# Optimization experiments

Hardware: AMD Instinct MI355X
Metric: run time of the kernel (lower is better)

Reference implementation:

```python
import jax, jax.numpy as jnp
import numpy as np

N = 50000
E = 800000
F_IN = 128
HID = 128
H_HID = 4
H_OUT = 6
N_CLS = 40
NEG_SLOPE = 0.2
BN_EPS = 1e-5


def gat_conv(x, src, dst, W, a_src, a_dst, bias, concat):
    # x: [N, F_in]; W: [F_in, H*C]; a_src/a_dst: [H, C]
    H, C = a_src.shape
    h = (x @ W).reshape(N, H, C)                      # [N,H,C]
    alpha_s = jnp.sum(h * a_src[None], axis=-1)       # [N,H]
    alpha_d = jnp.sum(h * a_dst[None], axis=-1)       # [N,H]
    e = jax.nn.leaky_relu(alpha_s[src] + alpha_d[dst], NEG_SLOPE)  # [E',H]
    # segment softmax over incoming edges of each dst node
    emax = jax.ops.segment_max(e, dst, num_segments=N)
    e = jnp.exp(e - emax[dst])
    denom = jax.ops.segment_sum(e, dst, num_segments=N)
    alpha = e / (denom[dst] + 1e-16)                  # [E',H]
    out = jax.ops.segment_sum(alpha[:, :, None] * h[src], dst, num_segments=N)  # [N,H,C]
    out = out.reshape(N, H * C) if concat else out.mean(axis=1)
    return out + bias


def bn_eval(x, gamma, beta, mean, var):
    return (x - mean) * (gamma / jnp.sqrt(var + BN_EPS)) + beta


def setup_inputs() -> dict:
    key = jax.random.key(0)
    ks = jax.random.split(key, 24)
    d_h = HID * H_HID  # 512
    inp = {
        'x': jax.random.normal(ks[0], (N, F_IN), jnp.float32),
        'edge_index': jax.random.randint(ks[1], (2, E), 0, N, jnp.int64),
        # layer 0: GATConv(128 -> 128, heads=4, concat)
        'W0': jax.random.normal(ks[2], (F_IN, d_h), jnp.float32) * 0.1,
        'as0': jax.random.normal(ks[3], (H_HID, HID), jnp.float32) * 0.1,
        'ad0': jax.random.normal(ks[4], (H_HID, HID), jnp.float32) * 0.1,
        'b0': jnp.zeros((d_h,), jnp.float32),
        'g0': jax.random.uniform(ks[5], (d_h,), jnp.float32, 0.5, 1.5),
        'bt0': jax.random.normal(ks[6], (d_h,), jnp.float32) * 0.1,
        'm0': jax.random.normal(ks[7], (d_h,), jnp.float32) * 0.1,
        'v0': jax.random.uniform(ks[8], (d_h,), jnp.float32, 0.5, 1.5),
        # layer 1: GATConv(512 -> 128, heads=4, concat)
        'W1': jax.random.normal(ks[9], (d_h, d_h), jnp.float32) * 0.05,
        'as1': jax.random.normal(ks[10], (H_HID, HID), jnp.float32) * 0.1,
        'ad1': jax.random.normal(ks[11], (H_HID, HID), jnp.float32) * 0.1,
        'b1': jnp.zeros((d_h,), jnp.float32),
        'g1': jax.random.uniform(ks[12], (d_h,), jnp.float32, 0.5, 1.5),
        'bt1': jax.random.normal(ks[13], (d_h,), jnp.float32) * 0.1,
        'm1': jax.random.normal(ks[14], (d_h,), jnp.float32) * 0.1,
        'v1': jax.random.uniform(ks[15], (d_h,), jnp.float32, 0.5, 1.5),
        # layer 2: GATConv(512 -> 40, heads=6, concat=False)
        'W2': jax.random.normal(ks[16], (d_h, H_OUT * N_CLS), jnp.float32) * 0.05,
        'as2': jax.random.normal(ks[17], (H_OUT, N_CLS), jnp.float32) * 0.1,
        'ad2': jax.random.normal(ks[18], (H_OUT, N_CLS), jnp.float32) * 0.1,
        'b2': jnp.zeros((N_CLS,), jnp.float32),
    }
    return inp


def reference(x, edge_index, W0, as0, ad0, b0, g0, bt0, m0, v0,
              W1, as1, ad1, b1, g1, bt1, m1, v1,
              W2, as2, ad2, b2):
    # add self loops (PyG GATConv default add_self_loops=True)
    loop = jnp.arange(N, dtype=edge_index.dtype)
    src = jnp.concatenate([edge_index[0], loop])
    dst = jnp.concatenate([edge_index[1], loop])
    # dropout is a no-op in eval mode
    h = gat_conv(x, src, dst, W0, as0, ad0, b0, concat=True)
    h = jax.nn.elu(bn_eval(h, g0, bt0, m0, v0))
    h = gat_conv(h, src, dst, W1, as1, ad1, b1, concat=True)
    h = jax.nn.elu(bn_eval(h, g1, bt1, m1, v1))
    h = gat_conv(h, src, dst, W2, as2, ad2, b2, concat=False)
    return jax.nn.log_softmax(h, axis=-1)
```

## Files before the change

### kernel.cpp

```cpp
#include <hip/hip_runtime.h>
#include <cstdint>
#include <cstddef>

#define NN 50000
#define EE 800000
#define EPQ (EE + NN)
#define NEG_SLOPE 0.2f
#define BN_EPS 1e-5f
#define SCB 256
#define NBLK ((NN + SCB - 1) / SCB)

typedef _Float16 f16x8 __attribute__((ext_vector_type(8)));
typedef _Float16 f16x4 __attribute__((ext_vector_type(4)));
typedef _Float16 f16x2 __attribute__((ext_vector_type(2)));
typedef float f32x4 __attribute__((ext_vector_type(4)));
typedef float f32x2 __attribute__((ext_vector_type(2)));
typedef unsigned int u32;
typedef unsigned char u8;
typedef unsigned short u16;

static __device__ __forceinline__ float lrelu(float x) { return x > 0.f ? x : x * NEG_SLOPE; }
static __device__ __forceinline__ int rfl(int v) { return __builtin_amdgcn_readfirstlane(v); }

static __device__ __forceinline__ u8 f32_to_fp8(float v) {
    return (u8)(__builtin_amdgcn_cvt_pk_fp8_f32(v, v, 0, false) & 0xff);
}
static __device__ __forceinline__ void fp8x4_to_f32(u32 v, float* o) {
    f32x2 lo = __builtin_amdgcn_cvt_pk_f32_fp8(v, false);
    f32x2 hi = __builtin_amdgcn_cvt_pk_f32_fp8(v, true);
    o[0] = lo[0]; o[1] = lo[1]; o[2] = hi[0]; o[3] = hi[1];
}

static __device__ __forceinline__ void gld_lds16(const void* g, void* l) {
    __builtin_amdgcn_global_load_lds((const __attribute__((address_space(1))) u32*)g,
                                     (__attribute__((address_space(3))) u32*)l, 16, 0, 0);
}

__global__ void hist_kernel(const int* __restrict__ dst, int* __restrict__ count) {
    int e = blockIdx.x * blockDim.x + threadIdx.x;
    if (e < EE) atomicAdd(&count[dst[e]], 1);
}

__global__ __launch_bounds__(SCB) void scan1(const int* __restrict__ count,
                                             int* __restrict__ excl, int* __restrict__ bsum) {
    __shared__ int tmp[SCB];
    int b = blockIdx.x, t = threadIdx.x;
    int i = b * SCB + t;
    int v = (i < NN) ? count[i] + 1 : 0;
    tmp[t] = v;
    __syncthreads();
    for (int off = 1; off < SCB; off <<= 1) {
        int u = (t >= off) ? tmp[t - off] : 0;
        __syncthreads();
        tmp[t] += u;
        __syncthreads();
    }
    if (i < NN) excl[i] = tmp[t] - v;
    if (t == SCB - 1) bsum[b] = tmp[t];
}

__global__ __launch_bounds__(256) void scan23(const int* __restrict__ excl,
                                              const int* __restrict__ bsum,
                                              int* __restrict__ rowptr, int* __restrict__ cursor) {
    __shared__ int pre[256];
    int t = threadIdx.x;
    int v = (t < NBLK) ? bsum[t] : 0;
    pre[t] = v;
    __syncthreads();
    for (int off = 1; off < 256; off <<= 1) {
        int u = (t >= off) ? pre[t - off] : 0;
        __syncthreads();
        pre[t] += u;
        __syncthreads();
    }
    int i = blockIdx.x * blockDim.x + t;
    if (i < NN) {
        int blk = i / SCB;
        int r = excl[i] + pre[blk] - ((blk < NBLK) ? bsum[blk] : 0);
        rowptr[i] = r;
        cursor[i] = r;
    }
    if (i == NN) rowptr[NN] = EPQ;
}

__global__ void scatter_kernel(const int* __restrict__ src, const int* __restrict__ dst,
                               int* __restrict__ cursor, int* __restrict__ csrs) {
    int e = blockIdx.x * blockDim.x + threadIdx.x;
    if (e < EE) {
        int d = dst[e];
        int slot = atomicAdd(&cursor[d], 1);
        csrs[slot] = src[e];
    } else if (e < EPQ) {
        int i = e - EE;
        int slot = atomicAdd(&cursor[i], 1);
        csrs[slot] = i;
    }
}

__global__ __launch_bounds__(256) void tcast_all(const float* __restrict__ W0,
                                                 const float* __restrict__ W1,
                                                 const float* __restrict__ W2,
                                                 _Float16* __restrict__ W0t,
                                                 _Float16* __restrict__ W1t,
                                                 _Float16* __restrict__ W2t) {
    __shared__ float tile[32][33];
    int b = blockIdx.x;
    const float* W; _Float16* Wt; int K, Nc, bx, by;
    if (b < 64)       { W = W0; Wt = W0t; K = 128; Nc = 512; int q = b;       bx = q % 16, by = q / 16; }
    else if (b < 320) { W = W1; Wt = W1t; K = 512; Nc = 512; int q = b - 64;  bx = q % 16, by = q / 16; }
    else              { W = W2; Wt = W2t; K = 512; Nc = 240; int q = b - 320; bx = q % 8,  by = q / 8; }
    bx *= 32; by *= 32;
    int tx = threadIdx.x & 31, ty = threadIdx.x >> 5;
#pragma unroll
    for (int r = 0; r < 32; r += 8) {
        int k = by + ty + r, n = bx + tx;
        tile[ty + r][tx] = (k < K && n < Nc) ? W[(size_t)k * Nc + n] : 0.f;
    }
    __syncthreads();
#pragma unroll
    for (int r = 0; r < 32; r += 8) {
        int n = bx + ty + r, k = by + tx;
        if (n < Nc && k < K) Wt[(size_t)n * K + k] = (_Float16)tile[tx][ty + r];
    }
}

__global__ __launch_bounds__(1024) void prep_all(const float* g0, const float* bt0,
                                                 const float* m0, const float* v0, const float* b0,
                                                 const float* g1, const float* bt1,
                                                 const float* m1, const float* v1, const float* b1,
                                                 const _Float16* __restrict__ W0t,
                                                 const _Float16* __restrict__ W1t,
                                                 const _Float16* __restrict__ W2t,
                                                 const float* __restrict__ as0,
                                                 const float* __restrict__ ad0,
                                                 const float* __restrict__ as1,
                                                 const float* __restrict__ ad1,
                                                 const float* __restrict__ as2,
                                                 const float* __restrict__ ad2,
                                                 float* sc01, float* sh01, float* va0, float* va1,
                                                 float* va2) {
    int bid = blockIdx.x, t = threadIdx.x;
    if (bid == 0) {
        const float *g, *bt, *m, *v, *b;
        int c;
        if (t < 512) { g = g0; bt = bt0; m = m0; v = v0; b = b0; c = t; }
        else         { g = g1; bt = bt1; m = m1; v = v1; b = b1; c = t - 512; }
        float s = g[c] * rsqrtf(v[c] + BN_EPS);
        sc01[t] = s;
        sh01[t] = (b[c] - m[c]) * s + bt[c];
        return;
    }
    int vb = bid - 1;
    if (vb < 8) {
        if (t >= 128) return;
        int j = vb, h = j & 3;
        const float* a = (j < 4 ? as0 : ad0) + h * 128;
        float s = 0.f;
        for (int c = 0; c < 128; c++) s += (float)W0t[(size_t)(h * 128 + c) * 128 + t] * a[c];
        va0[j * 128 + t] = s;
    } else if (vb < 16) {
        if (t >= 512) return;
        int j = vb - 8, h = j & 3;
        const float* a = (j < 4 ? as1 : ad1) + h * 128;
        float s = 0.f;
        for (int c = 0; c < 128; c++) s += (float)W1t[(size_t)(h * 128 + c) * 512 + t] * a[c];
        va1[j * 512 + t] = s;
    } else {
        if (t >= 512) return;
        int j = vb - 16, h = j % 6;
        const float* a = (j < 6 ? as2 : ad2) + h * 40;
        float s = 0.f;
        for (int c = 0; c < 40; c++) s += (float)W2t[(size_t)(h * 40 + c) * 512 + t] * a[c];
        va2[j * 512 + t] = s;
    }
}

__global__ __launch_bounds__(256) void castx_alpha0(const float* __restrict__ x,
                                                    const float* __restrict__ va0,
                                                    u8* __restrict__ xq, float* __restrict__ asn,
                                                    float* __restrict__ adn) {
    int wid = threadIdx.x >> 6, lane = threadIdx.x & 63;
    int i = blockIdx.x * 4 + wid;
    if (i >= NN) return;
    f32x2 xv = *(const f32x2*)(x + (size_t)i * 128 + lane * 2);
    u32 q = __builtin_amdgcn_cvt_pk_fp8_f32(xv[0], xv[1], 0, false);
    *((u16*)(xq + (size_t)i * 128) + lane) = (u16)(q & 0xffff);
    float p[8];
#pragma unroll
    for (int j = 0; j < 8; j++) {
        f32x2 v = *(const f32x2*)(va0 + j * 128 + lane * 2);
        p[j] = xv[0] * v[0] + xv[1] * v[1];
    }
#pragma unroll
    for (int off = 32; off; off >>= 1)
#pragma unroll
        for (int j = 0; j < 8; j++) p[j] += __shfl_xor(p[j], off);
    if (lane == 0) {
        f32x4 o0 = {p[0], p[1], p[2], p[3]}, o1 = {p[4], p[5], p[6], p[7]};
        *(f32x4*)(asn + (size_t)i * 4) = o0;
        *(f32x4*)(adn + (size_t)i * 4) = o1;
    }
}

template <int TK, bool BD, bool EPI, int OT>
__global__ __launch_bounds__(256) void gemm_t(const _Float16* __restrict__ A, int lda,
                                              const _Float16* __restrict__ Bt,
                                              void* __restrict__ Cv, int ldc, int M, int Nc,
                                              const float* __restrict__ sc,
                                              const float* __restrict__ sh) {
    __shared__ __align__(16) _Float16 As[2][128 * 64];
    __shared__ __align__(16) _Float16 Bs[2][128 * 64];
    const int t = threadIdx.x;
    const int bm = blockIdx.x * 128;
    const int bn = blockIdx.y * 128;
    const int wid = t >> 6, lane = t & 63;
    const int wm = (wid >> 1) * 64, wn = (wid & 1) * 64;
    const int aoff = BD ? bn : 0;
    f32x4 acc[4][4] = {};
    constexpr int nsteps = TK >> 6;

    auto STAGE = [&](int buf, int k0) {
#pragma unroll
        for (int it = 0; it < 4; ++it) {
            int rbase = it * 32 + wid * 8;
            int row = rbase + (lane >> 3);
            int c8g = (lane & 7) ^ (row & 7);
            gld_lds16(A + (size_t)(bm + row) * lda + aoff + k0 + c8g * 8,
                      (char*)As[buf] + rbase * 128);
            gld_lds16(Bt + (size_t)(bn + row) * TK + k0 + c8g * 8, (char*)Bs[buf] + rbase * 128);
        }
    };

    STAGE(0, 0);
    __syncthreads();
#pragma unroll
    for (int s = 0; s < nsteps; ++s) {
        const int cur = s & 1;
        if (s + 1 < nsteps) STAGE(cur ^ 1, (s + 1) * 64);
#pragma unroll
        for (int ks = 0; ks < 2; ++ks) {
            f16x8 af[4], bf[4];
#pragma unroll
            for (int mi = 0; mi < 4; ++mi) {
                int row = wm + mi * 16 + (lane & 15);
                int c8 = (ks * 4 + (lane >> 4)) ^ (row & 7);
                af[mi] = *(const f16x8*)((const char*)As[cur] + row * 128 + c8 * 16);
            }
#pragma unroll
            for (int ni = 0; ni < 4; ++ni) {
                int row = wn + ni * 16 + (lane & 15);
                int c8 = (ks * 4 + (lane >> 4)) ^ (row & 7);
                bf[ni] = *(const f16x8*)((const char*)Bs[cur] + row * 128 + c8 * 16);
            }
#pragma unroll
            for (int mi = 0; mi < 4; ++mi)
#pragma unroll
                for (int ni = 0; ni < 4; ++ni)
                    acc[mi][ni] = __builtin_amdgcn_mfma_f32_16x16x32_f16(af[mi], bf[ni],
                                                                         acc[mi][ni], 0, 0, 0);
        }
        __syncthreads();
    }
    float scv[4], shv[4];
    if (EPI) {
#pragma unroll
        for (int ni = 0; ni < 4; ++ni) {
            int gcol = bn + wn + ni * 16 + (lane & 15);
            scv[ni] = sc[gcol];
            shv[ni] = sh[gcol];
        }
    }
#pragma unroll
    for (int mi = 0; mi < 4; ++mi) {
#pragma unroll
        for (int r = 0; r < 4; ++r) {
            int grow = bm + wm + mi * 16 + (lane >> 4) * 4 + r;
            if (grow < M) {
#pragma unroll
                for (int ni = 0; ni < 4; ++ni) {
                    int gcol = bn + wn + ni * 16 + (lane & 15);
                    if (gcol < Nc) {
                        float v = acc[mi][ni][r];
                        if (EPI) {
                            v = v * scv[ni] + shv[ni];
                            v = v > 0.f ? v : expm1f(v);
                        }
                        if constexpr (OT == 0) {
                            ((_Float16*)Cv)[(size_t)grow * ldc + gcol] = (_Float16)v;
                        } else {
                            ((u8*)Cv)[(size_t)grow * ldc + gcol] = f32_to_fp8(v);
                        }
                    }
                }
            }
        }
    }
}

template <int JH, int STR>
__global__ __launch_bounds__(256) void alpha12(const _Float16* __restrict__ feat,
                                               const float* __restrict__ va,
                                               float* __restrict__ asn, float* __restrict__ adn) {
    int wid = threadIdx.x >> 6, lane = threadIdx.x & 63;
    int i = blockIdx.x * 4 + wid;
    if (i >= NN) return;
    f16x8 x8 = *(const f16x8*)(feat + (size_t)i * 512 + lane * 8);
    float xf[8];
#pragma unroll
    for (int u = 0; u < 8; u++) xf[u] = (float)x8[u];
    float p[2 * JH];
#pragma unroll
    for (int j = 0; j < 2 * JH; j++) {
        const float* vr = va + j * 512 + lane * 8;
        f32x4 v0 = *(const f32x4*)vr;
        f32x4 v1 = *(const f32x4*)(vr + 4);
        p[j] = xf[0] * v0[0] + xf[1] * v0[1] + xf[2] * v0[2] + xf[3] * v0[3] +
               xf[4] * v1[0] + xf[5] * v1[1] + xf[6] * v1[2] + xf[7] * v1[3];
    }
#pragma unroll
    for (int off = 32; off; off >>= 1)
#pragma unroll
        for (int j = 0; j < 2 * JH; j++) p[j] += __shfl_xor(p[j], off);
    if (lane == 0) {
#pragma unroll
        for (int h = 0; h < JH; h++) {
            asn[(size_t)i * STR + h] = p[h];
            adn[(size_t)i * STR + h] = p[JH + h];
        }
    }
}

__global__ __launch_bounds__(256) void aggx(const u8* __restrict__ xq,
                                            const float* __restrict__ asn,
                                            const float* __restrict__ adn,
                                            const int* __restrict__ rowptr,
                                            const int* __restrict__ csr,
                                            _Float16* __restrict__ xa) {
    __shared__ __align__(8) _Float16 wsl[4][64][4];
    int wid = threadIdx.x >> 6, lane = threadIdx.x & 63;
    int i = blockIdx.x * 4 + wid;
    if (i >= NN) return;
    int start = rfl(rowptr[i]), end = rfl(rowptr[i + 1]);
    int deg = end - start;
    bool fastp = deg <= 64;
    f32x4 ad = *(const f32x4*)(adn + (size_t)i * 4);
    f32x4 m4, rd4;
    if (fastp) {
        bool v = lane < deg;
        int e = start + (v ? lane : 0);
        int s = csr[e];
        f32x4 a = *(const f32x4*)(asn + (size_t)s * 4);
        f32x4 sc4, mm, wv, dn;
#pragma unroll
        for (int j = 0; j < 4; j++) { sc4[j] = v ? lrelu(a[j] + ad[j]) : -1e30f; mm[j] = sc4[j]; }
#pragma unroll
        for (int off = 32; off; off >>= 1)
#pragma unroll
            for (int j = 0; j < 4; j++) mm[j] = fmaxf(mm[j], __shfl_xor(mm[j], off));
#pragma unroll
        for (int j = 0; j < 4; j++) { wv[j] = v ? __expf(sc4[j] - mm[j]) : 0.f; dn[j] = wv[j]; }
#pragma unroll
        for (int off = 32; off; off >>= 1)
#pragma unroll
            for (int j = 0; j < 4; j++) dn[j] += __shfl_xor(dn[j], off);
        f16x4 o;
#pragma unroll
        for (int j = 0; j < 4; j++) o[j] = (_Float16)(wv[j] / (dn[j] + 1e-16f));
        *(f16x4*)&wsl[wid][lane][0] = o;
    } else {
        f32x4 mm = {-1e30f, -1e30f, -1e30f, -1e30f};
        for (int e = start + lane; e < end; e += 64) {
            int s = csr[e];
            f32x4 a = *(const f32x4*)(asn + (size_t)s * 4);
#pragma unroll
            for (int j = 0; j < 4; j++) mm[j] = fmaxf(mm[j], lrelu(a[j] + ad[j]));
        }
#pragma unroll
        for (int off = 32; off; off >>= 1)
#pragma unroll
            for (int j = 0; j < 4; j++) mm[j] = fmaxf(mm[j], __shfl_xor(mm[j], off));
        f32x4 dn = {0.f, 0.f, 0.f, 0.f};
        for (int e = start + lane; e < end; e += 64) {
            int s = csr[e];
            f32x4 a = *(const f32x4*)(asn + (size_t)s * 4);
#pragma unroll
            for (int j = 0; j < 4; j++) dn[j] += __expf(lrelu(a[j] + ad[j]) - mm[j]);
        }
#pragma unroll
        for (int off = 32; off; off >>= 1)
#pragma unroll
            for (int j = 0; j < 4; j++) dn[j] += __shfl_xor(dn[j], off);
        m4 = mm;
#pragma unroll
        for (int j = 0; j < 4; j++) rd4[j] = 1.f / (dn[j] + 1e-16f);
    }
    const char* xb = (const char*)xq + lane * 2;
    float acc[8] = {};
    int e = start;
    auto getw = [&](int ee, int ss, float* w) {
        if (fastp) {
            f16x4 wv4 = *(const f16x4*)&wsl[wid][ee - start][0];
#pragma unroll
            for (int h = 0; h < 4; h++) w[h] = (float)wv4[h];
        } else {
#pragma unroll
            for (int h = 0; h < 4; h++)
                w[h] = __expf(lrelu(asn[(size_t)ss * 4 + h] + ad[h]) - m4[h]) * rd4[h];
        }
    };
    for (; e + 4 <= end; e += 4) {
        int4 sv = *(const int4*)(csr + e);
        int s0 = rfl(sv.x), s1 = rfl(sv.y), s2 = rfl(sv.z), s3 = rfl(sv.w);
        u16 pv0 = *(const u16*)(xb + (u32)s0 * 128u);
        u16 pv1 = *(const u16*)(xb + (u32)s1 * 128u);
        u16 pv2 = *(const u16*)(xb + (u32)s2 * 128u);
        u16 pv3 = *(const u16*)(xb + (u32)s3 * 128u);
        float w0[4], w1[4], w2[4], w3[4];
        getw(e, s0, w0); getw(e + 1, s1, w1); getw(e + 2, s2, w2); getw(e + 3, s3, w3);
        f32x2 q0 = __builtin_amdgcn_cvt_pk_f32_fp8((u32)pv0, false);
        f32x2 q1 = __builtin_amdgcn_cvt_pk_f32_fp8((u32)pv1, false);
        f32x2 q2 = __builtin_amdgcn_cvt_pk_f32_fp8((u32)pv2, false);
        f32x2 q3 = __builtin_amdgcn_cvt_pk_f32_fp8((u32)pv3, false);
#pragma unroll
        for (int h = 0; h < 4; h++) {
            acc[h * 2]     += w0[h] * q0[0] + w1[h] * q1[0] + w2[h] * q2[0] + w3[h] * q3[0];
            acc[h * 2 + 1] += w0[h] * q0[1] + w1[h] * q1[1] + w2[h] * q2[1] + w3[h] * q3[1];
        }
    }
    for (; e < end; e++) {
        int s = rfl(csr[e]);
        float w[4];
        getw(e, s, w);
        u16 pv = *(const u16*)(xb + (u32)s * 128u);
        f32x2 q = __builtin_amdgcn_cvt_pk_f32_fp8((u32)pv, false);
#pragma unroll
        for (int h = 0; h < 4; h++) {
            acc[h * 2] += w[h] * q[0];
            acc[h * 2 + 1] += w[h] * q[1];
        }
    }
#pragma unroll
    for (int h = 0; h < 4; h++) {
        f16x2 o;
        o[0] = (_Float16)acc[h * 2];
        o[1] = (_Float16)acc[h * 2 + 1];
        *(f16x2*)(xa + (size_t)i * 512 + h * 128 + lane * 2) = o;
    }
}

__global__ __launch_bounds__(256) void agg01(const u8* __restrict__ h,
                                             const float* __restrict__ asn,
                                             const float* __restrict__ adn,
                                             const int* __restrict__ rowptr,
                                             const int* __restrict__ csr,
                                             const float* __restrict__ sc,
                                             const float* __restrict__ sh,
                                             _Float16* __restrict__ out) {
    __shared__ __align__(8) _Float16 wsl[4][64][4];
    int wid = threadIdx.x >> 6, lane = threadIdx.x & 63;
    int i = blockIdx.x * 4 + wid;
    if (i >= NN) return;
    int start = rfl(rowptr[i]), end = rfl(rowptr[i + 1]);
    int deg = end - start;
    bool fastp = deg <= 64;
    f32x4 ad = *(const f32x4*)(adn + (size_t)i * 4);
    f32x4 m4, rd4;
    if (fastp) {
        bool v = lane < deg;
        int e = start + (v ? lane : 0);
        int s = csr[e];
        f32x4 a = *(const f32x4*)(asn + (size_t)s * 4);
        f32x4 sc4, mm, wv, dn;
#pragma unroll
        for (int j = 0; j < 4; j++) { sc4[j] = v ? lrelu(a[j] + ad[j]) : -1e30f; mm[j] = sc4[j]; }
#pragma unroll
        for (int off = 32; off; off >>= 1)
#pragma unroll
            for (int j = 0; j < 4; j++) mm[j] = fmaxf(mm[j], __shfl_xor(mm[j], off));
#pragma unroll
        for (int j = 0; j < 4; j++) { wv[j] = v ? __expf(sc4[j] - mm[j]) : 0.f; dn[j] = wv[j]; }
#pragma unroll
        for (int off = 32; off; off >>= 1)
#pragma unroll
            for (int j = 0; j < 4; j++) dn[j] += __shfl_xor(dn[j], off);
        f16x4 o;
#pragma unroll
        for (int j = 0; j < 4; j++) o[j] = (_Float16)(wv[j] / (dn[j] + 1e-16f));
        *(f16x4*)&wsl[wid][lane][0] = o;
    } else {
        f32x4 mm = {-1e30f, -1e30f, -1e30f, -1e30f};
        for (int e = start + lane; e < end; e += 64) {
            int s = csr[e];
            f32x4 a = *(const f32x4*)(asn + (size_t)s * 4);
#pragma unroll
            for (int j = 0; j < 4; j++) mm[j] = fmaxf(mm[j], lrelu(a[j] + ad[j]));
        }
#pragma unroll
        for (int off = 32; off; off >>= 1)
#pragma unroll
            for (int j = 0; j < 4; j++) mm[j] = fmaxf(mm[j], __shfl_xor(mm[j], off));
        f32x4 dn = {0.f, 0.f, 0.f, 0.f};
        for (int e = start + lane; e < end; e += 64) {
            int s = csr[e];
            f32x4 a = *(const f32x4*)(asn + (size_t)s * 4);
#pragma unroll
            for (int j = 0; j < 4; j++) dn[j] += __expf(lrelu(a[j] + ad[j]) - mm[j]);
        }
#pragma unroll
        for (int off = 32; off; off >>= 1)
#pragma unroll
            for (int j = 0; j < 4; j++) dn[j] += __shfl_xor(dn[j], off);
        m4 = mm;
#pragma unroll
        for (int j = 0; j < 4; j++) rd4[j] = 1.f / (dn[j] + 1e-16f);
    }
    int head = lane >> 4;
    const char* hb = (const char*)h + lane * 8;
    float acc0[8] = {}, acc1[8] = {};
    int e = start;
    for (; e + 2 <= end; e += 2) {
        int2 sv = *(const int2*)(csr + e);
        int s0 = rfl(sv.x), s1 = rfl(sv.y);
        float w0, w1;
        if (fastp) {
            w0 = (float)wsl[wid][e - start][head];
            w1 = (float)wsl[wid][e + 1 - start][head];
        } else {
            w0 = __expf(lrelu(asn[(size_t)s0 * 4 + head] + ad[head]) - m4[head]) * rd4[head];
            w1 = __expf(lrelu(asn[(size_t)s1 * 4 + head] + ad[head]) - m4[head]) * rd4[head];
        }
        uint2 p0 = *(const uint2*)(hb + (u32)s0 * 512u);
        uint2 p1 = *(const uint2*)(hb + (u32)s1 * 512u);
        float q0[8], q1[8];
        fp8x4_to_f32(p0.x, q0); fp8x4_to_f32(p0.y, q0 + 4);
        fp8x4_to_f32(p1.x, q1); fp8x4_to_f32(p1.y, q1 + 4);
#pragma unroll
        for (int j = 0; j < 8; j++) {
            acc0[j] += w0 * q0[j];
            acc1[j] += w1 * q1[j];
        }
    }
    if (e < end) {
        int s0 = rfl(csr[e]);
        float w0;
        if (fastp) w0 = (float)wsl[wid][e - start][head];
        else w0 = __expf(lrelu(asn[(size_t)s0 * 4 + head] + ad[head]) - m4[head]) * rd4[head];
        uint2 p0 = *(const uint2*)(hb + (u32)s0 * 512u);
        float q0[8];
        fp8x4_to_f32(p0.x, q0); fp8x4_to_f32(p0.y, q0 + 4);
#pragma unroll
        for (int j = 0; j < 8; j++) acc0[j] += w0 * q0[j];
    }
    int ch = lane * 8;
    f32x4 sc0 = *(const f32x4*)(sc + ch), sc1 = *(const f32x4*)(sc + ch + 4);
    f32x4 sh0 = *(const f32x4*)(sh + ch), sh1 = *(const f32x4*)(sh + ch + 4);
    f16x8 o;
#pragma unroll
    for (int j = 0; j < 8; j++) {
        float s = (j < 4) ? sc0[j] : sc1[j - 4];
        float b = (j < 4) ? sh0[j] : sh1[j - 4];
        float val = (acc0[j] + acc1[j]) * s + b;
        val = val > 0.f ? val : expm1f(val);
        o[j] = (_Float16)val;
    }
    *(f16x8*)(out + (size_t)i * 512 + ch) = o;
}

__global__ __launch_bounds__(256) void agg2f(const u8* __restrict__ h2,
                                             const float* __restrict__ asn,
                                             const float* __restrict__ adn,
                                             const int* __restrict__ rowptr,
                                             const int* __restrict__ csr,
                                             const float* __restrict__ b2,
                                             float* __restrict__ out) {
    __shared__ __align__(16) _Float16 wsl[4][64][8];
    __shared__ float sval[4][240];
    int wid = threadIdx.x >> 6, lane = threadIdx.x & 63;
    int i = blockIdx.x * 4 + wid;
    if (i < NN) {
        int start = rfl(rowptr[i]), end = rfl(rowptr[i + 1]);
        int deg = end - start;
        bool fastp = deg <= 64;
        f32x4 ad0 = *(const f32x4*)(adn + (size_t)i * 8);
        f32x4 ad1 = *(const f32x4*)(adn + (size_t)i * 8 + 4);
        float adh[6] = {ad0[0], ad0[1], ad0[2], ad0[3], ad1[0], ad1[1]};
        float m6[6], rd6[6];
        if (fastp) {
            bool v = lane < deg;
            int e = start + (v ? lane : 0);
            int s = csr[e];
            f32x4 x0 = *(const f32x4*)(asn + (size_t)s * 8);
            f32x4 x1 = *(const f32x4*)(asn + (size_t)s * 8 + 4);
            float av[6] = {x0[0], x0[1], x0[2], x0[3], x1[0], x1[1]};
            float sc6[6], mm[6], wv[6], dn[6];
#pragma unroll
            for (int j = 0; j < 6; j++) {
                sc6[j] = v ? lrelu(av[j] + adh[j]) : -1e30f;
                mm[j] = sc6[j];
            }
#pragma unroll
            for (int off = 32; off; off >>= 1)
#pragma unroll
                for (int j = 0; j < 6; j++) mm[j] = fmaxf(mm[j], __shfl_xor(mm[j], off));
#pragma unroll
            for (int j = 0; j < 6; j++) { wv[j] = v ? __expf(sc6[j] - mm[j]) : 0.f; dn[j] = wv[j]; }
#pragma unroll
            for (int off = 32; off; off >>= 1)
#pragma unroll
                for (int j = 0; j < 6; j++) dn[j] += __shfl_xor(dn[j], off);
            f16x8 o;
#pragma unroll
            for (int j = 0; j < 6; j++) o[j] = (_Float16)(wv[j] / (dn[j] + 1e-16f));
            o[6] = (_Float16)0.f;
            o[7] = (_Float16)0.f;
            *(f16x8*)&wsl[wid][lane][0] = o;
        } else {
            float mm[6], dn[6];
#pragma unroll
            for (int j = 0; j < 6; j++) { mm[j] = -1e30f; dn[j] = 0.f; }
            for (int e = start + lane; e < end; e += 64) {
                int s = csr[e];
                f32x4 x0 = *(const f32x4*)(asn + (size_t)s * 8);
                f32x4 x1 = *(const f32x4*)(asn + (size_t)s * 8 + 4);
                float av[6] = {x0[0], x0[1], x0[2], x0[3], x1[0], x1[1]};
#pragma unroll
                for (int j = 0; j < 6; j++) mm[j] = fmaxf(mm[j], lrelu(av[j] + adh[j]));
            }
#pragma unroll
            for (int off = 32; off; off >>= 1)
#pragma unroll
                for (int j = 0; j < 6; j++) mm[j] = fmaxf(mm[j], __shfl_xor(mm[j], off));
            for (int e = start + lane; e < end; e += 64) {
                int s = csr[e];
                f32x4 x0 = *(const f32x4*)(asn + (size_t)s * 8);
                f32x4 x1 = *(const f32x4*)(asn + (size_t)s * 8 + 4);
                float av[6] = {x0[0], x0[1], x0[2], x0[3], x1[0], x1[1]};
#pragma unroll
                for (int j = 0; j < 6; j++) dn[j] += __expf(lrelu(av[j] + adh[j]) - mm[j]);
            }
#pragma unroll
            for (int off = 32; off; off >>= 1)
#pragma unroll
                for (int j = 0; j < 6; j++) dn[j] += __shfl_xor(dn[j], off);
#pragma unroll
            for (int j = 0; j < 6; j++) { m6[j] = mm[j]; rd6[j] = 1.f / (dn[j] + 1e-16f); }
        }
        int head = (lane < 60) ? (lane / 10) : 0;
        const char* hb = (const char*)h2 + lane * 4;
        float a0[4] = {}, a1[4] = {};
        int e = start;
        auto getw1 = [&](int ee, int ss) -> float {
            if (fastp) return (float)wsl[wid][ee - start][head];
            return __expf(lrelu(asn[(size_t)ss * 8 + head] + adh[head]) - m6[head]) * rd6[head];
        };
        for (; e + 4 <= end; e += 4) {
            int4 sv = *(const int4*)(csr + e);
            int s0 = rfl(sv.x), s1 = rfl(sv.y), s2 = rfl(sv.z), s3 = rfl(sv.w);
            u32 p0 = *(const u32*)(hb + (u32)s0 * 256u);
            u32 p1 = *(const u32*)(hb + (u32)s1 * 256u);
            u32 p2 = *(const u32*)(hb + (u32)s2 * 256u);
            u32 p3 = *(const u32*)(hb + (u32)s3 * 256u);
            float w0 = getw1(e, s0), w1 = getw1(e + 1, s1);
            float w2 = getw1(e + 2, s2), w3 = getw1(e + 3, s3);
            float q0[4], q1[4], q2[4], q3[4];
            fp8x4_to_f32(p0, q0);
            fp8x4_to_f32(p1, q1);
            fp8x4_to_f32(p2, q2);
            fp8x4_to_f32(p3, q3);
#pragma unroll
            for (int j = 0; j < 4; j++) {
                a0[j] += w0 * q0[j] + w2 * q2[j];
                a1[j] += w1 * q1[j] + w3 * q3[j];
            }
        }
        for (; e < end; e++) {
            int s0 = rfl(csr[e]);
            float w0 = getw1(e, s0);
            u32 p0 = *(const u32*)(hb + (u32)s0 * 256u);
            float q0[4];
            fp8x4_to_f32(p0, q0);
#pragma unroll
            for (int j = 0; j < 4; j++) a0[j] += w0 * q0[j];
        }
        if (lane < 60) {
#pragma unroll
            for (int j = 0; j < 4; j++) sval[wid][lane * 4 + j] = a0[j] + a1[j];
        }
    }
    __syncthreads();
    if (i < NN) {
        float v = -INFINITY;
        if (lane < 40) {
            float s = 0.f;
#pragma unroll
            for (int hh = 0; hh < 6; hh++) s += sval[wid][hh * 40 + lane];
            v = s * (1.0f / 6.0f) + b2[lane];
        }
        float mm = v;
#pragma unroll
        for (int off = 32; off; off >>= 1) mm = fmaxf(mm, __shfl_xor(mm, off));
        float se = (lane < 40) ? __expf(v - mm) : 0.f;
#pragma unroll
        for (int off = 32; off; off >>= 1) se += __shfl_xor(se, off);
        if (lane < 40) out[(size_t)i * 40 + lane] = v - mm - logf(se);
    }
}

extern "C" void kernel_launch(void* const* d_in, const int* in_sizes, int n_in,
                              void* d_out, int out_size, void* d_ws, size_t ws_size,
                              hipStream_t stream) {
    const float* x   = (const float*)d_in[0];
    const int*   ei  = (const int*)d_in[1];
    const float* W0  = (const float*)d_in[2];
    const float* as0 = (const float*)d_in[3];
    const float* ad0 = (const float*)d_in[4];
    const float* b0  = (const float*)d_in[5];
    const float* g0  = (const float*)d_in[6];
    const float* bt0 = (const float*)d_in[7];
    const float* m0  = (const float*)d_in[8];
    const float* v0  = (const float*)d_in[9];
    const float* W1  = (const float*)d_in[10];
    const float* as1 = (const float*)d_in[11];
    const float* ad1 = (const float*)d_in[12];
    const float* b1  = (const float*)d_in[13];
    const float* g1  = (const float*)d_in[14];
    const float* bt1 = (const float*)d_in[15];
    const float* m1  = (const float*)d_in[16];
    const float* v1  = (const float*)d_in[17];
    const float* W2  = (const float*)d_in[18];
    const float* as2w = (const float*)d_in[19];
    const float* ad2w = (const float*)d_in[20];
    const float* b2  = (const float*)d_in[21];
    float* out = (float*)d_out;
    const int* srcv = ei;
    const int* dstv = ei + EE;

    char* w = (char*)d_ws;
    auto carve = [&](size_t bytes) {
        char* p = w;
        w += (bytes + 255) & ~(size_t)255;
        return p;
    };
    u32* xq        = (u32*)carve((size_t)NN * 128);
    _Float16* hA   = (_Float16*)carve((size_t)NN * 512 * 2);
    _Float16* actB = (_Float16*)carve((size_t)NN * 512 * 2);
    _Float16* W0t  = (_Float16*)carve((size_t)512 * 128 * 2);
    _Float16* W1t  = (_Float16*)carve((size_t)512 * 512 * 2);
    _Float16* W2t  = (_Float16*)carve((size_t)240 * 512 * 2);
    float* va0  = (float*)carve((size_t)8 * 128 * 4);
    float* va1  = (float*)carve((size_t)8 * 512 * 4);
    float* va2  = (float*)carve((size_t)12 * 512 * 4);
    float* sc01 = (float*)carve((size_t)1024 * 4);
    float* sh01 = (float*)carve((size_t)1024 * 4);
    float* asn  = (float*)carve((size_t)NN * 8 * 4);
    float* adn  = (float*)carve((size_t)NN * 8 * 4);
    int* count  = (int*)carve((size_t)(NN + 8) * 4);
    int* excl   = (int*)carve((size_t)(NN + 8) * 4);
    int* bsum   = (int*)carve((size_t)512 * 4);
    int* rowptr = (int*)carve((size_t)(NN + 8) * 4);
    int* cursor = (int*)carve((size_t)(NN + 8) * 4);
    int* csrs   = (int*)carve((size_t)(EPQ + 8) * 4);
    _Float16* xa = hA;
    u8* h1q  = (u8*)hA;
    u8* h2q  = (u8*)hA;

    hipMemsetAsync(count, 0, (size_t)NN * 4, stream);
    hist_kernel<<<(EE + 255) / 256, 256, 0, stream>>>(dstv, count);
    scan1<<<NBLK, SCB, 0, stream>>>(count, excl, bsum);
    scan23<<<(NN + 256) / 256, 256, 0, stream>>>(excl, bsum, rowptr, cursor);
    scatter_kernel<<<(EPQ + 255) / 256, 256, 0, stream>>>(srcv, dstv, cursor, csrs);

    tcast_all<<<448, 256, 0, stream>>>(W0, W1, W2, W0t, W1t, W2t);
    prep_all<<<29, 1024, 0, stream>>>(g0, bt0, m0, v0, b0, g1, bt1, m1, v1, b1, W0t, W1t, W2t,
                                      as0, ad0, as1, ad1, as2w, ad2w, sc01, sh01, va0, va1, va2);

    const int MT = (NN + 127) / 128;
    const int NG = (NN + 3) / 4;

    castx_alpha0<<<NG, 256, 0, stream>>>(x, va0, (u8*)xq, asn, adn);
    aggx<<<NG, 256, 0, stream>>>((const u8*)xq, asn, adn, rowptr, csrs, xa);
    gemm_t<128, true, true, 0><<<dim3(MT, 4), 256, 0, stream>>>(xa, 512, W0t, actB, 512, NN, 512,
                                                                sc01, sh01);

    gemm_t<512, false, false, 1><<<dim3(MT, 4), 256, 0, stream>>>(actB, 512, W1t, h1q, 512, NN,
                                                                  512, nullptr, nullptr);
    alpha12<4, 4><<<NG, 256, 0, stream>>>(actB, va1, asn, adn);
    agg01<<<NG, 256, 0, stream>>>(h1q, asn, adn, rowptr, csrs, sc01 + 512, sh01 + 512, actB);

    gemm_t<512, false, false, 1><<<dim3(MT, 2), 256, 0, stream>>>(actB, 512, W2t, h2q, 256, NN,
                                                                  240, nullptr, nullptr);
    alpha12<6, 8><<<NG, 256, 0, stream>>>(actB, va2, asn, adn);
    agg2f<<<NG, 256, 0, stream>>>(h2q, asn, adn, rowptr, csrs, b2, out);
}
```

Baseline: 527.5 us.

## Fuse attention-logit dot products into GEMM and aggregation epilogues

Removes the two standalone alpha12 kernels. For layer 1, the attention logits are now computed in the epilogue of the layer-0 GEMM from fp32 pre-rounding values: each column tile reduces partial dot products across its lanes and atomically adds them into zeroed buffers. For layer 2, they are computed in the agg01 epilogue from the finished activations. This drops a full re-read of the 50000x512 fp16 activation twice and two kernel launches, at the cost of extra registers and atomics in the GEMM epilogue and a larger memset.

```diff
diff --git a/kernel.cpp b/kernel.cpp
--- a/kernel.cpp
+++ b/kernel.cpp
@@ -202,12 +202,15 @@
     }
 }
 
-template <int TK, bool BD, bool EPI, int OT>
+template <int TK, bool BD, bool EPI, int OT, bool AL>
 __global__ __launch_bounds__(256) void gemm_t(const _Float16* __restrict__ A, int lda,
                                               const _Float16* __restrict__ Bt,
                                               void* __restrict__ Cv, int ldc, int M, int Nc,
                                               const float* __restrict__ sc,
-                                              const float* __restrict__ sh) {
+                                              const float* __restrict__ sh,
+                                              const float* __restrict__ va,
+                                              float* __restrict__ asnO,
+                                              float* __restrict__ adnO) {
     __shared__ __align__(16) _Float16 As[2][128 * 64];
     __shared__ __align__(16) _Float16 Bs[2][128 * 64];
     const int t = threadIdx.x;
@@ -270,12 +273,21 @@
             shv[ni] = sh[gcol];
         }
     }
+    float vaj[8][4];
+    if (AL) {
+#pragma unroll
+        for (int j = 0; j < 8; ++j)
+#pragma unroll
+            for (int ni = 0; ni < 4; ++ni)
+                vaj[j][ni] = va[j * 512 + bn + wn + ni * 16 + (lane & 15)];
+    }
 #pragma unroll
     for (int mi = 0; mi < 4; ++mi) {
 #pragma unroll
         for (int r = 0; r < 4; ++r) {
             int grow = bm + wm + mi * 16 + (lane >> 4) * 4 + r;
             if (grow < M) {
+                float pj[8] = {};
 #pragma unroll
                 for (int ni = 0; ni < 4; ++ni) {
                     int gcol = bn + wn + ni * 16 + (lane & 15);
@@ -290,42 +302,26 @@
                         } else {
                             ((u8*)Cv)[(size_t)grow * ldc + gcol] = f32_to_fp8(v);
                         }
+                        if (AL) {
+#pragma unroll
+                            for (int j = 0; j < 8; ++j) pj[j] += v * vaj[j][ni];
+                        }
+                    }
+                }
+                if (AL) {
+#pragma unroll
+                    for (int off = 1; off < 16; off <<= 1)
+#pragma unroll
+                        for (int j = 0; j < 8; ++j) pj[j] += __shfl_xor(pj[j], off);
+                    if ((lane & 15) == 0) {
+#pragma unroll
+                        for (int j = 0; j < 4; ++j) {
+                            atomicAdd(&asnO[(size_t)grow * 4 + j], pj[j]);
+                            atomicAdd(&adnO[(size_t)grow * 4 + j], pj[4 + j]);
+                        }
                     }
                 }
             }
-        }
-    }
-}
-
-template <int JH, int STR>
-__global__ __launch_bounds__(256) void alpha12(const _Float16* __restrict__ feat,
-                                               const float* __restrict__ va,
-                                               float* __restrict__ asn, float* __restrict__ adn) {
-    int wid = threadIdx.x >> 6, lane = threadIdx.x & 63;
-    int i = blockIdx.x * 4 + wid;
-    if (i >= NN) return;
-    f16x8 x8 = *(const f16x8*)(feat + (size_t)i * 512 + lane * 8);
-    float xf[8];
-#pragma unroll
-    for (int u = 0; u < 8; u++) xf[u] = (float)x8[u];
-    float p[2 * JH];
-#pragma unroll
-    for (int j = 0; j < 2 * JH; j++) {
-        const float* vr = va + j * 512 + lane * 8;
-        f32x4 v0 = *(const f32x4*)vr;
-        f32x4 v1 = *(const f32x4*)(vr + 4);
-        p[j] = xf[0] * v0[0] + xf[1] * v0[1] + xf[2] * v0[2] + xf[3] * v0[3] +
-               xf[4] * v1[0] + xf[5] * v1[1] + xf[6] * v1[2] + xf[7] * v1[3];
-    }
-#pragma unroll
-    for (int off = 32; off; off >>= 1)
-#pragma unroll
-        for (int j = 0; j < 2 * JH; j++) p[j] += __shfl_xor(p[j], off);
-    if (lane == 0) {
-#pragma unroll
-        for (int h = 0; h < JH; h++) {
-            asn[(size_t)i * STR + h] = p[h];
-            adn[(size_t)i * STR + h] = p[JH + h];
         }
     }
 }
@@ -455,7 +451,10 @@
                                              const int* __restrict__ csr,
                                              const float* __restrict__ sc,
                                              const float* __restrict__ sh,
-                                             _Float16* __restrict__ out) {
+                                             const float* __restrict__ va2,
+                                             _Float16* __restrict__ out,
+                                             float* __restrict__ asnC,
+                                             float* __restrict__ adnC) {
     __shared__ __align__(8) _Float16 wsl[4][64][4];
     int wid = threadIdx.x >> 6, lane = threadIdx.x & 63;
     int i = blockIdx.x * 4 + wid;
@@ -555,15 +554,37 @@
     f32x4 sc0 = *(const f32x4*)(sc + ch), sc1 = *(const f32x4*)(sc + ch + 4);
     f32x4 sh0 = *(const f32x4*)(sh + ch), sh1 = *(const f32x4*)(sh + ch + 4);
     f16x8 o;
+    float valf[8];
 #pragma unroll
     for (int j = 0; j < 8; j++) {
         float s = (j < 4) ? sc0[j] : sc1[j - 4];
         float b = (j < 4) ? sh0[j] : sh1[j - 4];
         float val = (acc0[j] + acc1[j]) * s + b;
         val = val > 0.f ? val : expm1f(val);
+        valf[j] = val;
         o[j] = (_Float16)val;
     }
     *(f16x8*)(out + (size_t)i * 512 + ch) = o;
+    float pj[12];
+#pragma unroll
+    for (int j = 0; j < 12; j++) {
+        const float* vr = va2 + j * 512 + ch;
+        f32x4 v0 = *(const f32x4*)vr;
+        f32x4 v1 = *(const f32x4*)(vr + 4);
+        pj[j] = valf[0] * v0[0] + valf[1] * v0[1] + valf[2] * v0[2] + valf[3] * v0[3] +
+                valf[4] * v1[0] + valf[5] * v1[1] + valf[6] * v1[2] + valf[7] * v1[3];
+    }
+#pragma unroll
+    for (int off = 32; off; off >>= 1)
+#pragma unroll
+        for (int j = 0; j < 12; j++) pj[j] += __shfl_xor(pj[j], off);
+    if (lane == 0) {
+#pragma unroll
+        for (int hh = 0; hh < 6; hh++) {
+            asnC[(size_t)i * 8 + hh] = pj[hh];
+            adnC[(size_t)i * 8 + hh] = pj[6 + hh];
+        }
+    }
 }
 
 __global__ __launch_bounds__(256) void agg2f(const u8* __restrict__ h2,
@@ -752,9 +773,13 @@
     float* va2  = (float*)carve((size_t)12 * 512 * 4);
     float* sc01 = (float*)carve((size_t)1024 * 4);
     float* sh01 = (float*)carve((size_t)1024 * 4);
-    float* asn  = (float*)carve((size_t)NN * 8 * 4);
-    float* adn  = (float*)carve((size_t)NN * 8 * 4);
+    float* asnA = (float*)carve((size_t)NN * 4 * 4);
+    float* adnA = (float*)carve((size_t)NN * 4 * 4);
+    float* asnB = (float*)carve((size_t)NN * 4 * 4);
+    float* adnB = (float*)carve((size_t)NN * 4 * 4);
     int* count  = (int*)carve((size_t)(NN + 8) * 4);
+    float* asnC = (float*)carve((size_t)NN * 8 * 4);
+    float* adnC = (float*)carve((size_t)NN * 8 * 4);
     int* excl   = (int*)carve((size_t)(NN + 8) * 4);
     int* bsum   = (int*)carve((size_t)512 * 4);
     int* rowptr = (int*)carve((size_t)(NN + 8) * 4);
@@ -764,7 +789,9 @@
     u8* h1q  = (u8*)hA;
     u8* h2q  = (u8*)hA;
 
-    hipMemsetAsync(count, 0, (size_t)NN * 4, stream);
+    size_t zbytes = ((size_t)NN * 16 + 255 & ~(size_t)255) * 2 + (size_t)(NN + 8) * 4;
+    hipMemsetAsync(asnB, 0, zbytes, stream);
+
     hist_kernel<<<(EE + 255) / 256, 256, 0, stream>>>(dstv, count);
     scan1<<<NBLK, SCB, 0, stream>>>(count, excl, bsum);
     scan23<<<(NN + 256) / 256, 256, 0, stream>>>(excl, bsum, rowptr, cursor);
@@ -777,18 +804,17 @@
     const int MT = (NN + 127) / 128;
     const int NG = (NN + 3) / 4;
 
-    castx_alpha0<<<NG, 256, 0, stream>>>(x, va0, (u8*)xq, asn, adn);
-    aggx<<<NG, 256, 0, stream>>>((const u8*)xq, asn, adn, rowptr, csrs, xa);
-    gemm_t<128, true, true, 0><<<dim3(MT, 4), 256, 0, stream>>>(xa, 512, W0t, actB, 512, NN, 512,
-                                                                sc01, sh01);
-
-    gemm_t<512, false, false, 1><<<dim3(MT, 4), 256, 0, stream>>>(actB, 512, W1t, h1q, 512, NN,
-                                                                  512, nullptr, nullptr);
-    alpha12<4, 4><<<NG, 256, 0, stream>>>(actB, va1, asn, adn);
-    agg01<<<NG, 256, 0, stream>>>(h1q, asn, adn, rowptr, csrs, sc01 + 512, sh01 + 512, actB);
-
-    gemm_t<512, false, false, 1><<<dim3(MT, 2), 256, 0, stream>>>(actB, 512, W2t, h2q, 256, NN,
-                                                                  240, nullptr, nullptr);
-    alpha12<6, 8><<<NG, 256, 0, stream>>>(actB, va2, asn, adn);
-    agg2f<<<NG, 256, 0, stream>>>(h2q, asn, adn, rowptr, csrs, b2, out);
-}
+    castx_alpha0<<<NG, 256, 0, stream>>>(x, va0, (u8*)xq, asnA, adnA);
+    aggx<<<NG, 256, 0, stream>>>((const u8*)xq, asnA, adnA, rowptr, csrs, xa);
+    gemm_t<128, true, true, 0, true><<<dim3(MT, 4), 256, 0, stream>>>(
+        xa, 512, W0t, actB, 512, NN, 512, sc01, sh01, va1, asnB, adnB);
+
+    gemm_t<512, false, false, 1, false><<<dim3(MT, 4), 256, 0, stream>>>(
+        actB, 512, W1t, h1q, 512, NN, 512, nullptr, nullptr, nullptr, nullptr, nullptr);
+    agg01<<<NG, 256, 0, stream>>>(h1q, asnB, adnB, rowptr, csrs, sc01 + 512, sh01 + 512, va2,
+                                  actB, asnC, adnC);
+
+    gemm_t<512, false, false, 1, false><<<dim3(MT, 2), 256, 0, stream>>>(
+        actB, 512, W2t, h2q, 256, NN, 240, nullptr, nullptr, nullptr, nullptr, nullptr);
+    agg2f<<<NG, 256, 0, stream>>>(h2q, asnC, adnC, rowptr, csrs, b2, out);
+}
```

Result: slower. 654.1 us (+24.0%).
